# Performance work log

Hardware: AMD Instinct MI355X
Metric: run time of the kernel (lower is better)

Reference implementation:

```python
import jax, jax.numpy as jnp
import numpy as np

EPS = 1e-12


def _gather_neighbors(t, idx):
    # t: (bs, v, d), idx: (bs, v, n) -> (bs, v, n, d)  [torch: t[arange(bs)[:,None,None], idx]]
    bs, v, n = idx.shape
    flat = jnp.take_along_axis(t, idx.reshape(bs, v * n)[..., None], axis=1)
    return flat.reshape(bs, v, n, t.shape[-1])


def setup_inputs() -> dict:
    key = jax.random.key(0)
    ks = jax.random.split(key, 9)
    bs, v, n, inc, outc, sup = 8, 2048, 20, 64, 128, 2
    return {
        "neighbor_index": jax.random.randint(ks[0], (bs, v, n), 0, v),
        "vertices": jax.random.normal(ks[1], (bs, v, 3), dtype=jnp.float32),
        "feature_map": jax.random.normal(ks[2], (bs, v, inc), dtype=jnp.float32),
        "weights": jax.random.normal(ks[3], (inc, (sup + 1) * outc), dtype=jnp.float32) * 0.05,
        "bias": jax.random.normal(ks[4], ((sup + 1) * outc,), dtype=jnp.float32) * 0.05,
        "directions": jax.random.normal(ks[5], (3, sup * outc), dtype=jnp.float32) * 0.05,
        "distance_w": jax.random.normal(ks[6], (1, sup * outc), dtype=jnp.float32) * 0.05,
        "mlp_w": jax.random.normal(ks[7], (outc, 2 * outc), dtype=jnp.float32) * 0.05,
        "mlp_b": jax.random.normal(ks[8], (outc,), dtype=jnp.float32) * 0.05,
    }


def reference(neighbor_index, vertices, feature_map, weights, bias, directions, distance_w, mlp_w, mlp_b):
    bs, v, n = neighbor_index.shape
    outc = mlp_w.shape[0]
    sup = directions.shape[1] // outc

    # neighbor directions and distances (single gather, reuse norm)
    neighbors = _gather_neighbors(vertices, neighbor_index)          # (bs,v,n,3)
    direction = neighbors - vertices[:, :, None, :]                  # (bs,v,n,3)
    dist = jnp.linalg.norm(direction, axis=-1)                       # (bs,v,n)
    dir_norm = direction / jnp.maximum(dist[..., None], EPS)         # F.normalize
    dist_max = jnp.max(dist, axis=2, keepdims=True)                  # (bs,v,1)

    # support directions normalized along dim 0
    sdn = directions / jnp.maximum(jnp.linalg.norm(directions, axis=0, keepdims=True), EPS)
    theta = jax.nn.relu(jnp.einsum('bvnc,cs->bvns', dir_norm, sdn))  # (bs,v,n,sup*outc)
    dist_feat = jax.nn.relu(dist_max @ distance_w)                   # (bs,v,sup*outc)

    feat = feature_map @ weights + bias                              # (bs,v,(sup+1)*outc)
    center = feat[..., :outc]
    support = feat[..., outc:]
    support_g = _gather_neighbors(support, neighbor_index)           # (bs,v,n,sup*outc)

    act = (theta * support_g).reshape(bs, v, n, sup, outc)
    act = jnp.sum(jnp.max(act, axis=2), axis=2)                      # max over neighbors, sum over supports
    fuse = center + act                                              # (bs,v,outc)
    dist_sum = jnp.sum(dist_feat.reshape(bs, v, sup, outc), axis=2)  # (bs,v,outc)

    out = jnp.concatenate([fuse, dist_sum], axis=-1)                 # (bs,v,2*outc)
    return out @ mlp_w.T + mlp_b                                     # (bs,v,outc)
```

## Files before the change

### kernel.cpp

```cpp
#include <hip/hip_runtime.h>
#include <hip/hip_bf16.h>

#define BS    8
#define V     2048
#define NNB   20
#define INC   64
#define OUTC  128
#define SUP   2
#define NCOL  ((SUP + 1) * OUTC)
#define SCOL  (SUP * OUTC)
#define ROWS  (BS * V)

using bf16x8 = __bf16 __attribute__((ext_vector_type(8)));
using bf16x4 = __bf16 __attribute__((ext_vector_type(4)));
using f32x4  = float  __attribute__((ext_vector_type(4)));
using f32x2  = float  __attribute__((ext_vector_type(2)));
using i32x4  = int    __attribute__((ext_vector_type(4)));

#if __has_builtin(__builtin_elementwise_fma)
static __device__ inline f32x2 efma(f32x2 a, f32x2 b, f32x2 c) { return __builtin_elementwise_fma(a, b, c); }
#else
static __device__ inline f32x2 efma(f32x2 a, f32x2 b, f32x2 c) {
    f32x2 r; r[0] = fmaf(a[0], b[0], c[0]); r[1] = fmaf(a[1], b[1], c[1]); return r;
}
#endif
#if __has_builtin(__builtin_elementwise_max)
static __device__ inline f32x2 emax(f32x2 a, f32x2 b) { return __builtin_elementwise_max(a, b); }
#else
static __device__ inline f32x2 emax(f32x2 a, f32x2 b) {
    f32x2 r; r[0] = fmaxf(a[0], b[0]); r[1] = fmaxf(a[1], b[1]); return r;
}
#endif

static __device__ inline bf16x8 cvt8(f32x4 lo, f32x4 hi) {
    bf16x8 r;
    r[0] = (__bf16)lo[0]; r[1] = (__bf16)lo[1]; r[2] = (__bf16)lo[2]; r[3] = (__bf16)lo[3];
    r[4] = (__bf16)hi[0]; r[5] = (__bf16)hi[1]; r[6] = (__bf16)hi[2]; r[7] = (__bf16)hi[3];
    return r;
}

__global__ __launch_bounds__(256) void k_prep(const float* __restrict__ W,
                                              const float* __restrict__ Wm,
                                              const float* __restrict__ dw,
                                              __bf16* __restrict__ WTb,
                                              __bf16* __restrict__ Wm1b,
                                              float* __restrict__ w2) {
    const int b = blockIdx.x;
    if (b < 96) {
        const int idx = b * 256 + threadIdx.x;
        const int c = idx >> 6, k = idx & 63;
        WTb[idx] = (__bf16)W[k * NCOL + c];
    } else if (b < 160) {
        const int idx = (b - 96) * 256 + threadIdx.x;
        const int o = idx >> 7, k = idx & 127;
        Wm1b[idx] = (__bf16)Wm[o * SCOL + k];
    } else {
        __shared__ float u[OUTC];
        const int t = threadIdx.x;
        if (t < OUTC) u[t] = fmaxf(dw[t], 0.f) + fmaxf(dw[OUTC + t], 0.f);
        __syncthreads();
        if (t < OUTC) {
            float s = 0.f;
            for (int k = 0; k < OUTC; ++k) s = fmaf(Wm[t * SCOL + OUTC + k], u[k], s);
            w2[t] = s;
        }
    }
}

__global__ __launch_bounds__(256) void k_feat(const float* __restrict__ fm,
                                              const __bf16* __restrict__ WTb,
                                              const float* __restrict__ bias,
                                              float* __restrict__ center,
                                              float* __restrict__ support) {
    const int row0 = blockIdx.x * 32;
    const int wid = threadIdx.x >> 6, lane = threadIdx.x & 63;
    const int ln = lane & 15, lg = lane >> 4;
    const int cbase = wid * 96;

    bf16x8 a[2][2];
#pragma unroll
    for (int rs = 0; rs < 2; ++rs) {
        const float* ap = fm + (size_t)(row0 + rs * 16 + ln) * INC + lg * 8;
        a[rs][0] = cvt8(*(const f32x4*)(ap +  0), *(const f32x4*)(ap +  4));
        a[rs][1] = cvt8(*(const f32x4*)(ap + 32), *(const f32x4*)(ap + 36));
    }

    f32x4 acc[2][6];
#pragma unroll
    for (int t = 0; t < 6; ++t) {
        const float bb = bias[cbase + t * 16 + ln];
        acc[0][t] = (f32x4){bb, bb, bb, bb};
        acc[1][t] = acc[0][t];
    }

    const __bf16* bp = WTb + (size_t)(cbase + ln) * INC + lg * 8;
#pragma unroll
    for (int t = 0; t < 6; ++t) {
        const bf16x8 b0 = *(const bf16x8*)(bp + t * 16 * INC);
        const bf16x8 b1 = *(const bf16x8*)(bp + t * 16 * INC + 32);
        acc[0][t] = __builtin_amdgcn_mfma_f32_16x16x32_bf16(a[0][0], b0, acc[0][t], 0, 0, 0);
        acc[0][t] = __builtin_amdgcn_mfma_f32_16x16x32_bf16(a[0][1], b1, acc[0][t], 0, 0, 0);
        acc[1][t] = __builtin_amdgcn_mfma_f32_16x16x32_bf16(a[1][0], b0, acc[1][t], 0, 0, 0);
        acc[1][t] = __builtin_amdgcn_mfma_f32_16x16x32_bf16(a[1][1], b1, acc[1][t], 0, 0, 0);
    }

#pragma unroll
    for (int rs = 0; rs < 2; ++rs) {
        const int r0 = row0 + rs * 16 + lg * 4;
#pragma unroll
        for (int t = 0; t < 6; ++t) {
            const int col = cbase + t * 16 + ln;
            if (col < OUTC) {
#pragma unroll
                for (int r = 0; r < 4; ++r)
                    center[(size_t)(r0 + r) * OUTC + col] = acc[rs][t][r];
            } else {
                const int sc = col - OUTC;
#pragma unroll
                for (int r = 0; r < 4; ++r)
                    support[(size_t)(r0 + r) * SCOL + sc] = acc[rs][t][r];
            }
        }
    }
}

__global__ __launch_bounds__(256) void k_neigh(const int*   __restrict__ nbr,
                                               const float* __restrict__ verts,
                                               const float* __restrict__ dirs,
                                               const float* __restrict__ center,
                                               const float* __restrict__ support,
                                               __bf16* __restrict__ Xb,
                                               float* __restrict__ dmaxv) {
    const int bid   = blockIdx.x;
    const int batch = bid & 7;
    const int chunk = bid >> 3;
    const int wid   = threadIdx.x >> 6;
    const int lane  = threadIdx.x & 63;
    const int half  = lane >> 5;
    const int sl    = lane & 31;
    const int u     = chunk * 8 + wid * 2 + half;
    const int bV    = batch * V;
    const int row   = bV + u;
    const int c0    = sl * 4;

    f32x4 A0 = *(const f32x4*)(dirs +            c0);
    f32x4 A1 = *(const f32x4*)(dirs + SCOL +     c0);
    f32x4 A2 = *(const f32x4*)(dirs + 2*SCOL +   c0);
    f32x4 B0 = *(const f32x4*)(dirs +            OUTC + c0);
    f32x4 B1 = *(const f32x4*)(dirs + SCOL +     OUTC + c0);
    f32x4 B2 = *(const f32x4*)(dirs + 2*SCOL +   OUTC + c0);
#pragma unroll
    for (int j = 0; j < 4; ++j) {
        float inv = __builtin_amdgcn_rsqf(fmaxf(fmaf(A0[j], A0[j], fmaf(A1[j], A1[j], A2[j]*A2[j])), 1e-24f));
        A0[j] *= inv; A1[j] *= inv; A2[j] *= inv;
        inv = __builtin_amdgcn_rsqf(fmaxf(fmaf(B0[j], B0[j], fmaf(B1[j], B1[j], B2[j]*B2[j])), 1e-24f));
        B0[j] *= inv; B1[j] *= inv; B2[j] *= inv;
    }
    f32x2 ax0 = {A0[0], A0[1]}, ax1 = {A0[2], A0[3]};
    f32x2 ay0 = {A1[0], A1[1]}, ay1 = {A1[2], A1[3]};
    f32x2 az0 = {A2[0], A2[1]}, az1 = {A2[2], A2[3]};
    f32x2 bx0 = {B0[0], B0[1]}, bx1 = {B0[2], B0[3]};
    f32x2 by0 = {B1[0], B1[1]}, by1 = {B1[2], B1[3]};
    f32x2 bz0 = {B2[0], B2[1]}, bz1 = {B2[2], B2[3]};

    const float vx = verts[row * 3 + 0];
    const float vy = verts[row * 3 + 1];
    const float vz = verts[row * 3 + 2];

    int gs[NNB];
    {
        const i32x4* np4 = reinterpret_cast<const i32x4*>(nbr + (size_t)row * NNB);
#pragma unroll
        for (int t = 0; t < 5; ++t) {
            const i32x4 g4 = np4[t];
            gs[t*4+0] = g4[0]; gs[t*4+1] = g4[1]; gs[t*4+2] = g4[2]; gs[t*4+3] = g4[3];
        }
    }

    const f32x2 zero = {0.f, 0.f};
    f32x2 mA0 = {-INFINITY, -INFINITY}, mA1 = mA0, mB0 = mA0, mB1 = mA0;
    float d2max = 0.f;
    const float* supB = support + (size_t)bV * SCOL + c0;

#pragma unroll
    for (int j = 0; j < NNB; ++j) {
        const int g = bV + gs[j];
        const float px = verts[g * 3 + 0];
        const float py = verts[g * 3 + 1];
        const float pz = verts[g * 3 + 2];
        const float dx = px - vx, dy = py - vy, dz = pz - vz;
        const float d2 = fmaf(dx, dx, fmaf(dy, dy, dz * dz));
        d2max = fmaxf(d2max, d2);
        const float inv = __builtin_amdgcn_rsqf(fmaxf(d2, 1e-24f));
        const f32x2 nX = {dx * inv, dx * inv};
        const f32x2 nY = {dy * inv, dy * inv};
        const f32x2 nZ = {dz * inv, dz * inv};

        const float* sg = supB + (size_t)gs[j] * SCOL;
        const f32x4 s0 = *(const f32x4*)(sg);
        const f32x4 s1 = *(const f32x4*)(sg + OUTC);
        const f32x2 s0lo = {s0[0], s0[1]}, s0hi = {s0[2], s0[3]};
        const f32x2 s1lo = {s1[0], s1[1]}, s1hi = {s1[2], s1[3]};

        const f32x2 tA0 = emax(efma(nZ, az0, efma(nY, ay0, nX * ax0)), zero);
        const f32x2 tA1 = emax(efma(nZ, az1, efma(nY, ay1, nX * ax1)), zero);
        const f32x2 tB0 = emax(efma(nZ, bz0, efma(nY, by0, nX * bx0)), zero);
        const f32x2 tB1 = emax(efma(nZ, bz1, efma(nY, by1, nX * bx1)), zero);
        mA0 = emax(mA0, tA0 * s0lo);
        mA1 = emax(mA1, tA1 * s0hi);
        mB0 = emax(mB0, tB0 * s1lo);
        mB1 = emax(mB1, tB1 * s1hi);
    }

    const f32x4 cc = *(const f32x4*)(center + (size_t)row * OUTC + c0);
    const f32x2 f01 = (f32x2){cc[0], cc[1]} + mA0 + mB0;
    const f32x2 f23 = (f32x2){cc[2], cc[3]} + mA1 + mB1;
    bf16x4 fx;
    fx[0] = (__bf16)f01[0]; fx[1] = (__bf16)f01[1];
    fx[2] = (__bf16)f23[0]; fx[3] = (__bf16)f23[1];
    *(bf16x4*)(Xb + (size_t)row * OUTC + c0) = fx;
    if (sl == 0) dmaxv[row] = sqrtf(d2max);
}

__global__ __launch_bounds__(256) void k_out(const __bf16* __restrict__ Xb,
                                             const __bf16* __restrict__ Wm1b,
                                             const float* __restrict__ dmaxv,
                                             const float* __restrict__ w2,
                                             const float* __restrict__ mb,
                                             float* __restrict__ out) {
    const int wid = threadIdx.x >> 6, lane = threadIdx.x & 63;
    const int ln = lane & 15, lg = lane >> 4;
    const int row0 = blockIdx.x * 32 + (wid >> 1) * 16;
    const int cb = (wid & 1) * 64;

    const __bf16* ap = Xb + (size_t)(row0 + ln) * OUTC + lg * 8;
    bf16x8 a[4];
#pragma unroll
    for (int kf = 0; kf < 4; ++kf) a[kf] = *(const bf16x8*)(ap + kf * 32);

    f32x4 acc[4];
#pragma unroll
    for (int t = 0; t < 4; ++t) acc[t] = (f32x4)0.f;

    const __bf16* bp = Wm1b + (size_t)(cb + ln) * OUTC + lg * 8;
#pragma unroll
    for (int t = 0; t < 4; ++t) {
#pragma unroll
        for (int kf = 0; kf < 4; ++kf) {
            const bf16x8 b = *(const bf16x8*)(bp + t * 16 * OUTC + kf * 32);
            acc[t] = __builtin_amdgcn_mfma_f32_16x16x32_bf16(a[kf], b, acc[t], 0, 0, 0);
        }
    }

    float dm[4];
#pragma unroll
    for (int r = 0; r < 4; ++r) dm[r] = dmaxv[row0 + lg * 4 + r];

#pragma unroll
    for (int t = 0; t < 4; ++t) {
        const int col = cb + t * 16 + ln;
        const float w2c = w2[col];
        const float bb = mb[col];
#pragma unroll
        for (int r = 0; r < 4; ++r)
            out[(size_t)(row0 + lg * 4 + r) * OUTC + col] = fmaf(dm[r], w2c, acc[t][r] + bb);
    }
}

extern "C" void kernel_launch(void* const* d_in, const int* in_sizes, int n_in,
                              void* d_out, int out_size, void* d_ws, size_t ws_size,
                              hipStream_t stream) {
    const int*   nbr   = (const int*)  d_in[0];
    const float* verts = (const float*)d_in[1];
    const float* fm    = (const float*)d_in[2];
    const float* W     = (const float*)d_in[3];
    const float* bias  = (const float*)d_in[4];
    const float* dirs  = (const float*)d_in[5];
    const float* dw    = (const float*)d_in[6];
    const float* Wm    = (const float*)d_in[7];
    const float* mb    = (const float*)d_in[8];
    float* out = (float*)d_out;

    float*  center  = (float*)d_ws;
    float*  support = center + (size_t)ROWS * OUTC;
    __bf16* Xb      = (__bf16*)(support + (size_t)ROWS * SCOL);
    float*  dmaxv   = (float*)(Xb + (size_t)ROWS * OUTC);
    __bf16* WTb     = (__bf16*)(dmaxv + ROWS);
    __bf16* Wm1b    = WTb + NCOL * INC;
    float*  w2      = (float*)(Wm1b + OUTC * OUTC);

    k_prep <<<161,        256, 0, stream>>>(W, Wm, dw, WTb, Wm1b, w2);
    k_feat <<<ROWS / 32,  256, 0, stream>>>(fm, WTb, bias, center, support);
    k_neigh<<<ROWS / 8,   256, 0, stream>>>(nbr, verts, dirs, center, support, Xb, dmaxv);
    k_out  <<<ROWS / 32,  256, 0, stream>>>(Xb, Wm1b, dmaxv, w2, mb, out);
}
```

Baseline: 122.6 us.

## Store support features in bf16 and stage vertices in LDS for neighbor gather

```diff
diff --git a/kernel.cpp b/kernel.cpp
--- a/kernel.cpp
+++ b/kernel.cpp
@@ -16,6 +16,7 @@
 using f32x4  = float  __attribute__((ext_vector_type(4)));
 using f32x2  = float  __attribute__((ext_vector_type(2)));
 using i32x4  = int    __attribute__((ext_vector_type(4)));
+using u16x4  = unsigned short __attribute__((ext_vector_type(4)));
 
 #if __has_builtin(__builtin_elementwise_fma)
 static __device__ inline f32x2 efma(f32x2 a, f32x2 b, f32x2 c) { return __builtin_elementwise_fma(a, b, c); }
@@ -37,6 +38,10 @@
     r[0] = (__bf16)lo[0]; r[1] = (__bf16)lo[1]; r[2] = (__bf16)lo[2]; r[3] = (__bf16)lo[3];
     r[4] = (__bf16)hi[0]; r[5] = (__bf16)hi[1]; r[6] = (__bf16)hi[2]; r[7] = (__bf16)hi[3];
     return r;
+}
+
+static __device__ inline float b2f(unsigned short u) {
+    union { unsigned int i; float f; } c; c.i = ((unsigned int)u) << 16; return c.f;
 }
 
 __global__ __launch_bounds__(256) void k_prep(const float* __restrict__ W,
@@ -71,7 +76,7 @@
                                               const __bf16* __restrict__ WTb,
                                               const float* __restrict__ bias,
                                               float* __restrict__ center,
-                                              float* __restrict__ support) {
+                                              __bf16* __restrict__ supb) {
     const int row0 = blockIdx.x * 32;
     const int wid = threadIdx.x >> 6, lane = threadIdx.x & 63;
     const int ln = lane & 15, lg = lane >> 4;
@@ -118,19 +123,19 @@
                 const int sc = col - OUTC;
 #pragma unroll
                 for (int r = 0; r < 4; ++r)
-                    support[(size_t)(r0 + r) * SCOL + sc] = acc[rs][t][r];
+                    supb[(size_t)(r0 + r) * SCOL + sc] = (__bf16)acc[rs][t][r];
             }
         }
     }
 }
 
-__global__ __launch_bounds__(256) void k_neigh(const int*   __restrict__ nbr,
-                                               const float* __restrict__ verts,
-                                               const float* __restrict__ dirs,
-                                               const float* __restrict__ center,
-                                               const float* __restrict__ support,
-                                               __bf16* __restrict__ Xb,
-                                               float* __restrict__ dmaxv) {
+__global__ __launch_bounds__(256, 4) void k_neigh(const int*   __restrict__ nbr,
+                                                  const float* __restrict__ verts,
+                                                  const float* __restrict__ dirs,
+                                                  const float* __restrict__ center,
+                                                  const __bf16* __restrict__ supb,
+                                                  __bf16* __restrict__ Xb,
+                                                  float* __restrict__ dmaxv) {
     const int bid   = blockIdx.x;
     const int batch = bid & 7;
     const int chunk = bid >> 3;
@@ -143,6 +148,13 @@
     const int row   = bV + u;
     const int c0    = sl * 4;
 
+    __shared__ float vlds[V][4];
+
+    for (int i = threadIdx.x; i < V * 3; i += 256) {
+        const int vv = i / 3, cc = i - vv * 3;
+        vlds[vv][cc] = verts[(size_t)bV * 3 + i];
+    }
+
     f32x4 A0 = *(const f32x4*)(dirs +            c0);
     f32x4 A1 = *(const f32x4*)(dirs + SCOL +     c0);
     f32x4 A2 = *(const f32x4*)(dirs + 2*SCOL +   c0);
@@ -156,16 +168,13 @@
         inv = __builtin_amdgcn_rsqf(fmaxf(fmaf(B0[j], B0[j], fmaf(B1[j], B1[j], B2[j]*B2[j])), 1e-24f));
         B0[j] *= inv; B1[j] *= inv; B2[j] *= inv;
     }
-    f32x2 ax0 = {A0[0], A0[1]}, ax1 = {A0[2], A0[3]};
-    f32x2 ay0 = {A1[0], A1[1]}, ay1 = {A1[2], A1[3]};
-    f32x2 az0 = {A2[0], A2[1]}, az1 = {A2[2], A2[3]};
-    f32x2 bx0 = {B0[0], B0[1]}, bx1 = {B0[2], B0[3]};
-    f32x2 by0 = {B1[0], B1[1]}, by1 = {B1[2], B1[3]};
-    f32x2 bz0 = {B2[0], B2[1]}, bz1 = {B2[2], B2[3]};
-
-    const float vx = verts[row * 3 + 0];
-    const float vy = verts[row * 3 + 1];
-    const float vz = verts[row * 3 + 2];
+    const f32x2 ax0 = {A0[0], A0[1]}, ax1 = {A0[2], A0[3]};
+    const f32x2 ay0 = {A1[0], A1[1]}, ay1 = {A1[2], A1[3]};
+    const f32x2 az0 = {A2[0], A2[1]}, az1 = {A2[2], A2[3]};
+    const f32x2 bx0 = {B0[0], B0[1]}, bx1 = {B0[2], B0[3]};
+    const f32x2 by0 = {B1[0], B1[1]}, by1 = {B1[2], B1[3]};
+    const f32x2 bz0 = {B2[0], B2[1]}, bz1 = {B2[2], B2[3]};
+    const f32x2 zero = {0.f, 0.f};
 
     int gs[NNB];
     {
@@ -177,39 +186,50 @@
         }
     }
 
-    const f32x2 zero = {0.f, 0.f};
+    __syncthreads();
+
+    const float vx = vlds[u][0], vy = vlds[u][1], vz = vlds[u][2];
+
     f32x2 mA0 = {-INFINITY, -INFINITY}, mA1 = mA0, mB0 = mA0, mB1 = mA0;
     float d2max = 0.f;
-    const float* supB = support + (size_t)bV * SCOL + c0;
-
-#pragma unroll
-    for (int j = 0; j < NNB; ++j) {
-        const int g = bV + gs[j];
-        const float px = verts[g * 3 + 0];
-        const float py = verts[g * 3 + 1];
-        const float pz = verts[g * 3 + 2];
-        const float dx = px - vx, dy = py - vy, dz = pz - vz;
-        const float d2 = fmaf(dx, dx, fmaf(dy, dy, dz * dz));
-        d2max = fmaxf(d2max, d2);
-        const float inv = __builtin_amdgcn_rsqf(fmaxf(d2, 1e-24f));
-        const f32x2 nX = {dx * inv, dx * inv};
-        const f32x2 nY = {dy * inv, dy * inv};
-        const f32x2 nZ = {dz * inv, dz * inv};
-
-        const float* sg = supB + (size_t)gs[j] * SCOL;
-        const f32x4 s0 = *(const f32x4*)(sg);
-        const f32x4 s1 = *(const f32x4*)(sg + OUTC);
-        const f32x2 s0lo = {s0[0], s0[1]}, s0hi = {s0[2], s0[3]};
-        const f32x2 s1lo = {s1[0], s1[1]}, s1hi = {s1[2], s1[3]};
-
-        const f32x2 tA0 = emax(efma(nZ, az0, efma(nY, ay0, nX * ax0)), zero);
-        const f32x2 tA1 = emax(efma(nZ, az1, efma(nY, ay1, nX * ax1)), zero);
-        const f32x2 tB0 = emax(efma(nZ, bz0, efma(nY, by0, nX * bx0)), zero);
-        const f32x2 tB1 = emax(efma(nZ, bz1, efma(nY, by1, nX * bx1)), zero);
-        mA0 = emax(mA0, tA0 * s0lo);
-        mA1 = emax(mA1, tA1 * s0hi);
-        mB0 = emax(mB0, tB0 * s1lo);
-        mB1 = emax(mB1, tB1 * s1hi);
+    const __bf16* supBase = supb + (size_t)bV * SCOL + c0;
+
+#pragma unroll
+    for (int t = 0; t < 4; ++t) {
+        u16x4 s0r[5], s1r[5];
+        f32x4 vl[5];
+#pragma unroll
+        for (int q = 0; q < 5; ++q) {
+            const int g = gs[t * 5 + q];
+            const __bf16* sg = supBase + (size_t)g * SCOL;
+            s0r[q] = *(const u16x4*)(sg);
+            s1r[q] = *(const u16x4*)(sg + OUTC);
+            vl[q]  = *(const f32x4*)&vlds[g][0];
+        }
+#pragma unroll
+        for (int q = 0; q < 5; ++q) {
+            const float dx = vl[q][0] - vx, dy = vl[q][1] - vy, dz = vl[q][2] - vz;
+            const float d2 = fmaf(dx, dx, fmaf(dy, dy, dz * dz));
+            d2max = fmaxf(d2max, d2);
+            const float inv = __builtin_amdgcn_rsqf(fmaxf(d2, 1e-24f));
+            const f32x2 nX = {dx * inv, dx * inv};
+            const f32x2 nY = {dy * inv, dy * inv};
+            const f32x2 nZ = {dz * inv, dz * inv};
+
+            const f32x2 s0lo = {b2f(s0r[q][0]), b2f(s0r[q][1])};
+            const f32x2 s0hi = {b2f(s0r[q][2]), b2f(s0r[q][3])};
+            const f32x2 s1lo = {b2f(s1r[q][0]), b2f(s1r[q][1])};
+            const f32x2 s1hi = {b2f(s1r[q][2]), b2f(s1r[q][3])};
+
+            const f32x2 tA0 = emax(efma(nZ, az0, efma(nY, ay0, nX * ax0)), zero);
+            const f32x2 tA1 = emax(efma(nZ, az1, efma(nY, ay1, nX * ax1)), zero);
+            const f32x2 tB0 = emax(efma(nZ, bz0, efma(nY, by0, nX * bx0)), zero);
+            const f32x2 tB1 = emax(efma(nZ, bz1, efma(nY, by1, nX * bx1)), zero);
+            mA0 = emax(mA0, tA0 * s0lo);
+            mA1 = emax(mA1, tA1 * s0hi);
+            mB0 = emax(mB0, tB0 * s1lo);
+            mB1 = emax(mB1, tB1 * s1hi);
+        }
     }
 
     const f32x4 cc = *(const f32x4*)(center + (size_t)row * OUTC + c0);
@@ -282,15 +302,15 @@
     float* out = (float*)d_out;
 
     float*  center  = (float*)d_ws;
-    float*  support = center + (size_t)ROWS * OUTC;
-    __bf16* Xb      = (__bf16*)(support + (size_t)ROWS * SCOL);
+    __bf16* supb    = (__bf16*)(center + (size_t)ROWS * OUTC);
+    __bf16* Xb      = supb + (size_t)ROWS * SCOL;
     float*  dmaxv   = (float*)(Xb + (size_t)ROWS * OUTC);
     __bf16* WTb     = (__bf16*)(dmaxv + ROWS);
     __bf16* Wm1b    = WTb + NCOL * INC;
     float*  w2      = (float*)(Wm1b + OUTC * OUTC);
 
     k_prep <<<161,        256, 0, stream>>>(W, Wm, dw, WTb, Wm1b, w2);
-    k_feat <<<ROWS / 32,  256, 0, stream>>>(fm, WTb, bias, center, support);
-    k_neigh<<<ROWS / 8,   256, 0, stream>>>(nbr, verts, dirs, center, support, Xb, dmaxv);
+    k_feat <<<ROWS / 32,  256, 0, stream>>>(fm, WTb, bias, center, supb);
+    k_neigh<<<ROWS / 8,   256, 0, stream>>>(nbr, verts, dirs, center, supb, Xb, dmaxv);
     k_out  <<<ROWS / 32,  256, 0, stream>>>(Xb, Wm1b, dmaxv, w2, mb, out);
 }
```

Result: no change. 124.4 us (+1.5%).
